# Performance work log

Hardware: AMD Instinct MI355X
Metric: run time of the kernel (lower is better)

Reference implementation:

```python
import jax, jax.numpy as jnp
import numpy as np

HEADS = 8
KEY_DIM = 64
VALUE_DIM = 64


def setup_inputs() -> dict:
    key = jax.random.key(0)
    ks = jax.random.split(key, 6)
    B, I, O, T, S = 2, 512, 512, 2048, 2048
    E = KEY_DIM * HEADS  # 512
    Ev = VALUE_DIM * HEADS  # 512
    return {
        "x": jax.random.normal(ks[0], (B, I, T), dtype=jnp.float32),
        "y": jax.random.normal(ks[1], (B, O, S), dtype=jnp.float32),
        "mask": jnp.zeros((T, S), dtype=jnp.float32),
        "Wk": jax.random.normal(ks[2], (E, I), dtype=jnp.float32) * (I ** -0.5),
        "Wv": jax.random.normal(ks[3], (Ev, I), dtype=jnp.float32) * (I ** -0.5),
        "Wq": jax.random.normal(ks[4], (E, O), dtype=jnp.float32) * (O ** -0.5),
        "W": jax.random.normal(ks[5], (O, Ev), dtype=jnp.float32) * (Ev ** -0.5),
        "b": jnp.zeros((O,), dtype=jnp.float32),
    }


def reference(x, y, mask, Wk, Wv, Wq, W, b):
    B, I, T = x.shape
    S = y.shape[2]
    H, dk, dv = HEADS, KEY_DIM, VALUE_DIM
    scaling = dk ** -0.5
    # 1x1 Conv1d projections == channel GEMMs; reshape (B, H*d, L) -> (B*H, d, L)
    keys = jnp.einsum('ei,bit->bet', Wk, x).reshape(B * H, dk, T)
    values = jnp.einsum('ei,bit->bet', Wv, x).reshape(B * H, dv, T)
    queries = jnp.einsum('eo,bos->bes', Wq, y).reshape(B * H, dk, S)
    # scores: [B*H, T, S]
    dot = jnp.einsum('bkt,bks->bts', keys, queries)
    dot = dot + mask[None, :, :]
    # torch Softmax(1) on [bh, T, S] normalizes over T (keys axis);
    # note: scaling applied AFTER mask add, as in the original.
    attention = jax.nn.softmax(scaling * dot, axis=1)
    # weighted values: [B*H, dv, S] -> [B, H*dv, S]
    output = jnp.einsum('bvt,bts->bvs', values, attention).reshape(B, H * dv, S)
    # final Linear over channel dim applied to (B, S, H*dv)
    return jnp.einsum('bvs,ov->bso', output, W) + b
```

## Files before the change

kernel.cpp:

```cpp
#include <hip/hip_runtime.h>
#include <stdint.h>

typedef unsigned short u16;
typedef unsigned int u32;

#define B_    2
#define DK    64
#define T_    2048
#define S_    2048
#define CI    512
#define CO    512
#define E_    512

typedef short  short8 __attribute__((ext_vector_type(8)));
typedef __bf16 bf16x8 __attribute__((ext_vector_type(8)));
typedef float  f32x4  __attribute__((ext_vector_type(4)));

static __device__ __forceinline__ u16 f2bf(float f) {
    return __builtin_bit_cast(u16, (__bf16)f);
}

static __device__ __forceinline__ float bf2f(u16 h) {
    return __uint_as_float((u32)h << 16);
}

static __device__ __forceinline__ short8 ld8(const u16* p) {
    return *(const short8*)p;
}

static __device__ __forceinline__ f32x4 mfma_bf16(short8 a, short8 b, f32x4 c) {
    return __builtin_amdgcn_mfma_f32_16x16x32_bf16(
        __builtin_bit_cast(bf16x8, a), __builtin_bit_cast(bf16x8, b), c, 0, 0, 0);
}

__global__ __launch_bounds__(256) void k_prep(const float* __restrict__ x, const float* __restrict__ y,
                                              const float* __restrict__ wk, const float* __restrict__ wv,
                                              const float* __restrict__ wq, const float* __restrict__ wf,
                                              const float* __restrict__ mask,
                                              u16* __restrict__ xt, u16* __restrict__ yt,
                                              u16* __restrict__ wkb, u16* __restrict__ wvb,
                                              u16* __restrict__ wqb, u16* __restrict__ wfb,
                                              u16* __restrict__ mt, u32* __restrict__ mflag) {
    __shared__ float tile[64][65];
    int bid = blockIdx.x;
    if (bid < 1024) {
        int bx = bid & 31, by = (bid >> 5) & 7, bz = bid >> 8;
        int tsel = bz >> 1, b = bz & 1;
        const float* src = tsel ? y : x;
        u16* dst = tsel ? yt : xt;
        int t0 = bx * 64, i0 = by * 64;
        int tx = threadIdx.x & 15, ty = threadIdx.x >> 4;
#pragma unroll
        for (int r = 0; r < 4; r++) {
            int i = ty + r * 16;
            *(float4*)&tile[i][tx * 4] =
                *(const float4*)(src + (size_t)(b * CI + i0 + i) * T_ + t0 + tx * 4);
        }
        __syncthreads();
        int tx2 = threadIdx.x & 7, ty2 = threadIdx.x >> 3;
#pragma unroll
        for (int r = 0; r < 2; r++) {
            int t = ty2 + r * 32;
            short8 o;
#pragma unroll
            for (int j = 0; j < 8; j++)
                o[j] = (short)f2bf(tile[tx2 * 8 + j][t]);
            *(short8*)(dst + (size_t)(b * T_ + t0 + t) * CI + i0 + tx2 * 8) = o;
        }
    } else if (bid < 1536) {
        int off = ((bid - 1024) * 256 + threadIdx.x) * 8;
        int w = off >> 18, r = off & 262143;
        const float* s = (w == 0) ? wk : (w == 1) ? wv : (w == 2) ? wq : wf;
        u16* d = (w == 0) ? wkb : (w == 1) ? wvb : (w == 2) ? wqb : wfb;
        float4 a0 = *(const float4*)(s + r);
        float4 a1 = *(const float4*)(s + r + 4);
        short8 o;
        o[0] = f2bf(a0.x); o[1] = f2bf(a0.y); o[2] = f2bf(a0.z); o[3] = f2bf(a0.w);
        o[4] = f2bf(a1.x); o[5] = f2bf(a1.y); o[6] = f2bf(a1.z); o[7] = f2bf(a1.w);
        *(short8*)(d + r) = o;
    } else {
        int mb = bid - 1536;
        int bx = mb & 31, by = mb >> 5;
        int t0 = bx * 64, s0 = by * 64;
        int tx = threadIdx.x & 15, ty = threadIdx.x >> 4;
        const float msc = 0.125f * 1.44269504088896f;
        bool nz = false;
#pragma unroll
        for (int r = 0; r < 4; r++) {
            int t = ty + r * 16;
            float4 v = *(const float4*)(mask + (size_t)(t0 + t) * S_ + s0 + tx * 4);
            nz |= (v.x != 0.0f) | (v.y != 0.0f) | (v.z != 0.0f) | (v.w != 0.0f);
            *(float4*)&tile[t][tx * 4] = v;
        }
        if (mflag && __any(nz) && (threadIdx.x & 63) == 0)
            atomicOr(mflag, 1u);
        __syncthreads();
        int tx2 = threadIdx.x & 7, ty2 = threadIdx.x >> 3;
#pragma unroll
        for (int r = 0; r < 2; r++) {
            int s = ty2 + r * 32;
            short8 o;
#pragma unroll
            for (int j = 0; j < 8; j++)
                o[j] = (short)f2bf(tile[tx2 * 8 + j][s] * msc);
            *(short8*)(mt + (size_t)(s0 + s) * T_ + t0 + tx2 * 8) = o;
        }
    }
}

__global__ __launch_bounds__(256) void k_proj3(const u16* __restrict__ xt, const u16* __restrict__ yt,
                                               const u16* __restrict__ wkb, const u16* __restrict__ wvb,
                                               const u16* __restrict__ wqb,
                                               u16* __restrict__ ktd, u16* __restrict__ vtd,
                                               u16* __restrict__ qtd, int p_base) {
    int bi = blockIdx.x;
    int p = p_base + (bi >> 8);
    int r = bi & 255;
    int et = r & 3, tt = r >> 2;
    int wv = threadIdx.x >> 6, lane = threadIdx.x & 63;
    int col = lane & 15, q = lane >> 4;
    int b = tt >> 5;
    int t0 = (tt & 31) * 64 + (wv >> 1) * 32;
    int e0 = et * 128 + (wv & 1) * 64;
    const u16* src = (p == 0) ? yt : xt;
    const u16* wb  = (p == 0) ? wqb : (p == 1) ? wkb : wvb;
    const u16* ap0 = src + (size_t)(b * T_ + t0 + col) * CI + q * 8;
    const u16* bp0 = wb + (size_t)(e0 + col) * CI + q * 8;
    f32x4 acc[2][4] = {};
    short8 a0 = ld8(ap0), a1 = ld8(ap0 + 16 * CI);
    short8 b0 = ld8(bp0), b1 = ld8(bp0 + 16 * CI);
    short8 b2 = ld8(bp0 + 32 * CI), b3 = ld8(bp0 + 48 * CI);
#pragma unroll
    for (int ks = 0; ks < 16; ks++) {
        short8 na0, na1, nb0, nb1, nb2, nb3;
        if (ks < 15) {
            na0 = ld8(ap0 + (ks + 1) * 32);
            na1 = ld8(ap0 + 16 * CI + (ks + 1) * 32);
            nb0 = ld8(bp0 + (ks + 1) * 32);
            nb1 = ld8(bp0 + 16 * CI + (ks + 1) * 32);
            nb2 = ld8(bp0 + 32 * CI + (ks + 1) * 32);
            nb3 = ld8(bp0 + 48 * CI + (ks + 1) * 32);
        }
        acc[0][0] = mfma_bf16(a0, b0, acc[0][0]); acc[1][0] = mfma_bf16(a1, b0, acc[1][0]);
        acc[0][1] = mfma_bf16(a0, b1, acc[0][1]); acc[1][1] = mfma_bf16(a1, b1, acc[1][1]);
        acc[0][2] = mfma_bf16(a0, b2, acc[0][2]); acc[1][2] = mfma_bf16(a1, b2, acc[1][2]);
        acc[0][3] = mfma_bf16(a0, b3, acc[0][3]); acc[1][3] = mfma_bf16(a1, b3, acc[1][3]);
        if (ks < 15) {
            a0 = na0; a1 = na1; b0 = nb0; b1 = nb1; b2 = nb2; b3 = nb3;
        }
    }
    float qs = (p == 0) ? 0.180336880f : 1.0f;
    u16* dst = (p == 0) ? qtd : (p == 1) ? ktd : vtd;
    if (p < 2) {
#pragma unroll
        for (int mt = 0; mt < 2; mt++)
#pragma unroll
            for (int nt = 0; nt < 4; nt++) {
                int e = e0 + nt * 16 + col, h = e >> 6, k = e & 63;
                u16* dp = dst + ((size_t)(b * 8 + h) * T_ + t0 + mt * 16 + q * 4) * DK + k;
                dp[0] = f2bf(acc[mt][nt][0] * qs);
                dp[DK] = f2bf(acc[mt][nt][1] * qs);
                dp[2 * DK] = f2bf(acc[mt][nt][2] * qs);
                dp[3 * DK] = f2bf(acc[mt][nt][3] * qs);
            }
    } else {
#pragma unroll
        for (int mt = 0; mt < 2; mt++)
#pragma unroll
            for (int nt = 0; nt < 4; nt++) {
                int e = e0 + nt * 16 + col, h = e >> 6, v = e & 63;
                uint2 pk;
                pk.x = f2bf(acc[mt][nt][0]) | ((u32)f2bf(acc[mt][nt][1]) << 16);
                pk.y = f2bf(acc[mt][nt][2]) | ((u32)f2bf(acc[mt][nt][3]) << 16);
                *(uint2*)(dst + ((size_t)(b * 8 + h) * DK + v) * T_ + t0 + mt * 16 + q * 4) = pk;
            }
    }
}


#define ATTN_ITER_M(T0, KC, MC4, MCF, KN, MN4, MNF, TN)  do {                       \
    short8 vb0 = ld8(vbase + (T0));                                                 \
    short8 vb1 = ld8(vbase + 16 * (size_t)T_ + (T0));                               \
    short8 vb2 = ld8(vbase + 32 * (size_t)T_ + (T0));                               \
    short8 vb3 = ld8(vbase + 48 * (size_t)T_ + (T0));                               \
    f32x4 s0g[4], s1g[4];                                                           \
    __builtin_amdgcn_s_setprio(1);                                                  \
    _Pragma("unroll") for (int g = 0; g < 4; g++) {                                 \
        f32x4 z = {};                                                               \
        s0g[g] = mfma_bf16(KC[0], qa[g][0], z);                                     \
        s0g[g] = mfma_bf16(KC[1], qa[g][1], s0g[g]);                                \
        s1g[g] = mfma_bf16(KC[2], qa[g][0], z);                                     \
        s1g[g] = mfma_bf16(KC[3], qa[g][1], s1g[g]);                                \
    }                                                                               \
    __builtin_amdgcn_s_setprio(0);                                                  \
    KN[0] = ld8(kbase + (size_t)(TN) * DK);                                         \
    KN[1] = ld8(kbase + (size_t)(TN) * DK + 32);                                    \
    KN[2] = ld8(kbase + (size_t)((TN) + 4) * DK);                                   \
    KN[3] = ld8(kbase + (size_t)((TN) + 4) * DK + 32);                              \
    if constexpr (MODE == 1) {                                                      \
        _Pragma("unroll") for (int g = 0; g < 4; g++) {                             \
            MN4[g][0] = *(const ushort4*)(mtb[g] + (TN));                           \
            MN4[g][1] = *(const ushort4*)(mtb[g] + (TN) + 4);                       \
        }                                                                           \
    } else {                                                                        \
        _Pragma("unroll") for (int g = 0; g < 4; g++)                               \
        _Pragma("unroll") for (int st = 0; st < 2; st++)                            \
        _Pragma("unroll") for (int rr = 0; rr < 4; rr++)                            \
            MNF[g][st * 4 + rr] =                                                   \
                mbs[g][(size_t)((TN) + q * 8 + st * 4 + rr) * S_] * msc;            \
    }                                                                               \
    _Pragma("unroll") for (int g = 0; g < 4; g++) {                                 \
        bf16x8 pbv;                                                                 \
        float lsum = 0.f;                                                           \
        _Pragma("unroll") for (int i = 0; i < 8; i++) {                             \
            float sv = (i < 4) ? s0g[g][i & 3] : s1g[g][i & 3];                     \
            float mv;                                                               \
            if constexpr (MODE == 1)                                                \
                mv = bf2f(((const u16*)&MC4[g][i >> 2])[i & 3]);                    \
            else                                                                    \
                mv = MCF[g][i];                                                     \
            float p = __builtin_amdgcn_exp2f(sv + mv);                              \
            lsum += p;                                                              \
            pbv[i] = (__bf16)p;                                                     \
        }                                                                           \
        l_part[g] += lsum;                                                          \
        short8 pa = __builtin_bit_cast(short8, pbv);                                \
        __builtin_amdgcn_s_setprio(1);                                              \
        oacc[g][0] = mfma_bf16(vb0, pa, oacc[g][0]);                                \
        oacc[g][1] = mfma_bf16(vb1, pa, oacc[g][1]);                                \
        oacc[g][2] = mfma_bf16(vb2, pa, oacc[g][2]);                                \
        oacc[g][3] = mfma_bf16(vb3, pa, oacc[g][3]);                                \
        __builtin_amdgcn_s_setprio(0);                                              \
    }                                                                               \
} while (0)

#define ATTN_ITER_NM(T0, KC, KN, TN)  do {                                          \
    short8 vb0 = ld8(vbase + (T0));                                                 \
    short8 vb1 = ld8(vbase + 16 * (size_t)T_ + (T0));                               \
    short8 vb2 = ld8(vbase + 32 * (size_t)T_ + (T0));                               \
    short8 vb3 = ld8(vbase + 48 * (size_t)T_ + (T0));                               \
    f32x4 s0g[4], s1g[4];                                                           \
    __builtin_amdgcn_s_setprio(1);                                                  \
    _Pragma("unroll") for (int g = 0; g < 4; g++) {                                 \
        f32x4 z = {};                                                               \
        s0g[g] = mfma_bf16(KC[0], qa[g][0], z);                                     \
        s0g[g] = mfma_bf16(KC[1], qa[g][1], s0g[g]);                                \
        s1g[g] = mfma_bf16(KC[2], qa[g][0], z);                                     \
        s1g[g] = mfma_bf16(KC[3], qa[g][1], s1g[g]);                                \
    }                                                                               \
    __builtin_amdgcn_s_setprio(0);                                                  \
    KN[0] = ld8(kbase + (size_t)(TN) * DK);                                         \
    KN[1] = ld8(kbase + (size_t)(TN) * DK + 32);                                    \
    KN[2] = ld8(kbase + (size_t)((TN) + 4) * DK);                                   \
    KN[3] = ld8(kbase + (size_t)((TN) + 4) * DK + 32);                              \
    _Pragma("unroll") for (int g = 0; g < 4; g++) {                                 \
        bf16x8 pbv;                                                                 \
        float lsum = 0.f;                                                           \
        _Pragma("unroll") for (int i = 0; i < 8; i++) {                             \
            float sv = (i < 4) ? s0g[g][i & 3] : s1g[g][i & 3];                     \
            float p = __builtin_amdgcn_exp2f(sv);                                   \
            lsum += p;                                                              \
            pbv[i] = (__bf16)p;                                                     \
        }                                                                           \
        l_part[g] += lsum;                                                          \
        short8 pa = __builtin_bit_cast(short8, pbv);                                \
        __builtin_amdgcn_s_setprio(1);                                              \
        oacc[g][0] = mfma_bf16(vb0, pa, oacc[g][0]);                                \
        oacc[g][1] = mfma_bf16(vb1, pa, oacc[g][1]);                                \
        oacc[g][2] = mfma_bf16(vb2, pa, oacc[g][2]);                                \
        oacc[g][3] = mfma_bf16(vb3, pa, oacc[g][3]);                                \
        __builtin_amdgcn_s_setprio(0);                                              \
    }                                                                               \
} while (0)

template<int MODE>
__global__ __launch_bounds__(512, 2) void k_attn(const u16* __restrict__ kt, const u16* __restrict__ qt,
                                                 const u16* __restrict__ vt, const float* __restrict__ mask,
                                                 const u16* __restrict__ mt, const u32* __restrict__ mflag,
                                                 u16* __restrict__ oa) {
    __shared__ struct { float O[8][16][68]; float L[8][16]; } Sm;
    int wv = threadIdx.x >> 6, lane = threadIdx.x & 63;
    int col = lane & 15, q = lane >> 4;
    int bid = blockIdx.x;
    int j = bid >> 3;
    int bh = (bid & 7) * 2 + (j >> 5);
    int s_base = (j & 31) * 64;
    int sg = s_base + col;
    const int t_begin = wv * (T_ / 8);
    const int t_end = t_begin + (T_ / 8);
    short8 qa[4][2];
#pragma unroll
    for (int g = 0; g < 4; g++) {
        const u16* qp = qt + (size_t)(bh * S_ + sg + g * 16) * DK + q * 8;
        qa[g][0] = ld8(qp);
        qa[g][1] = ld8(qp + 32);
    }
    int tperm = ((col >> 2) << 3) | (col & 3);
    const u16* kbase = kt + (size_t)bh * T_ * DK + (size_t)tperm * DK + q * 8;
    const u16* vbase = vt + (size_t)bh * DK * T_ + (size_t)col * T_ + q * 8;
    float l_part[4] = {0.f, 0.f, 0.f, 0.f};
    f32x4 oacc[4][4] = {};
    const float msc = 0.180336880f;

    int use_mask = mflag ? (int)*mflag : 1;

    if (use_mask == 0) {
        short8 kA[4], kB[4];
        kA[0] = ld8(kbase + (size_t)t_begin * DK);
        kA[1] = ld8(kbase + (size_t)t_begin * DK + 32);
        kA[2] = ld8(kbase + (size_t)(t_begin + 4) * DK);
        kA[3] = ld8(kbase + (size_t)(t_begin + 4) * DK + 32);
        for (int t0 = t_begin; t0 < t_end; t0 += 64) {
            ATTN_ITER_NM(t0, kA, kB, t0 + 32);
            int tn2 = (t0 + 64 < t_end) ? (t0 + 64) : t_begin;
            ATTN_ITER_NM(t0 + 32, kB, kA, tn2);
        }
    } else {
        const float* mbs[4];
        const u16* mtb[4];
#pragma unroll
        for (int g = 0; g < 4; g++) {
            mbs[g] = mask + sg + g * 16;
            mtb[g] = mt + (size_t)(sg + g * 16) * T_ + q * 8;
        }
        short8 kA[4], kB[4];
        ushort4 mA4[4][2], mB4[4][2];
        float mAf[4][8], mBf[4][8];
        kA[0] = ld8(kbase + (size_t)t_begin * DK);
        kA[1] = ld8(kbase + (size_t)t_begin * DK + 32);
        kA[2] = ld8(kbase + (size_t)(t_begin + 4) * DK);
        kA[3] = ld8(kbase + (size_t)(t_begin + 4) * DK + 32);
        if constexpr (MODE == 1) {
#pragma unroll
            for (int g = 0; g < 4; g++) {
                mA4[g][0] = *(const ushort4*)(mtb[g] + t_begin);
                mA4[g][1] = *(const ushort4*)(mtb[g] + t_begin + 4);
            }
        } else {
#pragma unroll
            for (int g = 0; g < 4; g++)
#pragma unroll
                for (int st = 0; st < 2; st++)
#pragma unroll
                    for (int rr = 0; rr < 4; rr++)
                        mAf[g][st * 4 + rr] =
                            mbs[g][(size_t)(t_begin + q * 8 + st * 4 + rr) * S_] * msc;
        }
        for (int t0 = t_begin; t0 < t_end; t0 += 64) {
            ATTN_ITER_M(t0, kA, mA4, mAf, kB, mB4, mBf, t0 + 32);
            int tn2 = (t0 + 64 < t_end) ? (t0 + 64) : t_begin;
            ATTN_ITER_M(t0 + 32, kB, mB4, mBf, kA, mA4, mAf, tn2);
        }
    }

#pragma unroll
    for (int g = 0; g < 4; g++) {
        float lr = l_part[g];
        lr += __shfl_xor(lr, 16);
        lr += __shfl_xor(lr, 32);
        l_part[g] = lr;
    }

    int b = bh >> 3, h = bh & 7;
    __syncthreads();
#pragma unroll
    for (int g = 0; g < 4; g++) {
#pragma unroll
        for (int nt = 0; nt < 4; nt++)
            *(f32x4*)&Sm.O[wv][col][nt * 16 + q * 4] = oacc[g][nt];
        if (lane < 16)
            Sm.L[wv][lane] = l_part[g];
        __syncthreads();
#pragma unroll
        for (int e = 0; e < 2; e++) {
            int f = (int)threadIdx.x + e * 512;
            int s = f >> 6, v = f & 63;
            float acc = 0.f, lt = 0.f;
#pragma unroll
            for (int c = 0; c < 8; c++) {
                acc += Sm.O[c][s][v];
                lt += Sm.L[c][s];
            }
            oa[(size_t)(b * S_ + s_base + g * 16 + s) * E_ + h * DK + v] = f2bf(acc / lt);
        }
        __syncthreads();
    }
}

__global__ __launch_bounds__(256) void k_final(const u16* __restrict__ oa, const u16* __restrict__ wfb,
                                               const float* __restrict__ bias, float* __restrict__ out) {
    int bi = blockIdx.x;
    int et = bi & 7, tt = bi >> 3;
    int wv = threadIdx.x >> 6, lane = threadIdx.x & 63;
    int col = lane & 15, q = lane >> 4;
    int b = tt >> 5;
    int s0 = (tt & 31) * 64 + (wv >> 1) * 32;
    int o0 = et * 64 + (wv & 1) * 32;
    const u16* ap0 = oa + (size_t)(b * S_ + s0 + col) * E_ + q * 8;
    const u16* bp0 = wfb + (size_t)(o0 + col) * E_ + q * 8;
    f32x4 acc[2][2] = {};
    short8 a0 = ld8(ap0), a1 = ld8(ap0 + 16 * E_);
    short8 b0 = ld8(bp0), b1 = ld8(bp0 + 16 * E_);
#pragma unroll
    for (int ks = 0; ks < 16; ks++) {
        short8 na0, na1, nb0, nb1;
        if (ks < 15) {
            na0 = ld8(ap0 + (ks + 1) * 32);
            na1 = ld8(ap0 + 16 * E_ + (ks + 1) * 32);
            nb0 = ld8(bp0 + (ks + 1) * 32);
            nb1 = ld8(bp0 + 16 * E_ + (ks + 1) * 32);
        }
        acc[0][0] = mfma_bf16(a0, b0, acc[0][0]); acc[1][0] = mfma_bf16(a1, b0, acc[1][0]);
        acc[0][1] = mfma_bf16(a0, b1, acc[0][1]); acc[1][1] = mfma_bf16(a1, b1, acc[1][1]);
        if (ks < 15) {
            a0 = na0; a1 = na1; b0 = nb0; b1 = nb1;
        }
    }
#pragma unroll
    for (int mt = 0; mt < 2; mt++)
#pragma unroll
        for (int nt = 0; nt < 2; nt++) {
            int o = o0 + nt * 16 + col;
            float bn = bias[o];
#pragma unroll
            for (int r = 0; r < 4; r++) {
                int s = s0 + mt * 16 + q * 4 + r;
                out[(size_t)(b * S_ + s) * CO + o] = acc[mt][nt][r] + bn;
            }
        }
}

extern "C" void kernel_launch(void* const* d_in, const int* in_sizes, int n_in,
                              void* d_out, int out_size, void* d_ws, size_t ws_size,
                              hipStream_t stream) {
    const float* x    = (const float*)d_in[0];
    const float* y    = (const float*)d_in[1];
    const float* mask = (const float*)d_in[2];
    const float* Wk   = (const float*)d_in[3];
    const float* Wv   = (const float*)d_in[4];
    const float* Wq   = (const float*)d_in[5];
    const float* Wf   = (const float*)d_in[6];
    const float* bias = (const float*)d_in[7];
    float* out = (float*)d_out;

    u16* ws = (u16*)d_ws;
    u16* XT  = ws;
    u16* YT  = XT + 2097152;
    u16* WKB = YT + 2097152;
    u16* WVB = WKB + 262144;
    u16* WQB = WVB + 262144;
    u16* WFB = WQB + 262144;
    u16* KT  = WFB + 262144;
    u16* QT  = KT + 2097152;
    u16* MT  = QT + 2097152;
    u16* VTs = MT + 4194304;
    u32* MF  = (u32*)(VTs + 2097152);
    u16* OA  = XT;

    int use_mt   = (ws_size >= (size_t)27262976) ? 1 : 0;
    int has_vt   = (ws_size >= (size_t)31457280) ? 1 : 0;
    int has_flag = (ws_size >= (size_t)31457344) ? 1 : 0;
    u16* VT = has_vt ? VTs : YT;
    u32* MFp = (use_mt && has_flag) ? MF : (u32*)nullptr;

    if (MFp)
        hipMemsetAsync(MFp, 0, 4, stream);
    k_prep<<<use_mt ? 2560 : 1536, 256, 0, stream>>>(x, y, Wk, Wv, Wq, Wf, mask,
                                                     XT, YT, WKB, WVB, WQB, WFB, MT, MFp);
    if (has_vt) {
        k_proj3<<<768, 256, 0, stream>>>(XT, YT, WKB, WVB, WQB, KT, VT, QT, 0);
    } else {
        k_proj3<<<512, 256, 0, stream>>>(XT, YT, WKB, WVB, WQB, KT, VT, QT, 0);
        k_proj3<<<256, 256, 0, stream>>>(XT, YT, WKB, WVB, WQB, KT, VT, QT, 2);
    }
    if (use_mt)
        k_attn<1><<<512, 512, 0, stream>>>(KT, QT, VT, mask, MT, MFp, OA);
    else
        k_attn<0><<<512, 512, 0, stream>>>(KT, QT, VT, mask, MT, MFp, OA);
    k_final<<<512, 256, 0, stream>>>(OA, WFB, bias, out);
}
```

Measured before the change: 195.5 us.

## Store K and V in MFMA fragment-major layout for contiguous attention loads

The projection kernel now writes K and V in a pre-swizzled fragment layout: per 32-row t-tile and per 16-byte register fragment, all 64 lanes' data sit contiguously. The attention kernel then loads each K/V fragment as one fully coalesced 1 KB wave-wide read at lane*8, instead of strided per-row gathers with a tperm permutation. This is meant to cut memory transactions and address arithmetic in the attention inner loop. In exchange the projection kernel does scattered 2-byte stores for K and small uint2 stores for V into the swizzled layout.

```diff
diff --git a/kernel.cpp b/kernel.cpp
--- a/kernel.cpp
+++ b/kernel.cpp
@@ -111,7 +111,7 @@
 __global__ __launch_bounds__(256) void k_proj3(const u16* __restrict__ xt, const u16* __restrict__ yt,
                                                const u16* __restrict__ wkb, const u16* __restrict__ wvb,
                                                const u16* __restrict__ wqb,
-                                               u16* __restrict__ ktd, u16* __restrict__ vtd,
+                                               u16* __restrict__ kfd, u16* __restrict__ vfd,
                                                u16* __restrict__ qtd, int p_base) {
     int bi = blockIdx.x;
     int p = p_base + (bi >> 8);
@@ -149,40 +149,60 @@
             a0 = na0; a1 = na1; b0 = nb0; b1 = nb1; b2 = nb2; b3 = nb3;
         }
     }
-    float qs = (p == 0) ? 0.180336880f : 1.0f;
-    u16* dst = (p == 0) ? qtd : (p == 1) ? ktd : vtd;
-    if (p < 2) {
+    const float qs = 0.180336880f;
+    if (p == 0) {
 #pragma unroll
         for (int mt = 0; mt < 2; mt++)
 #pragma unroll
             for (int nt = 0; nt < 4; nt++) {
                 int e = e0 + nt * 16 + col, h = e >> 6, k = e & 63;
-                u16* dp = dst + ((size_t)(b * 8 + h) * T_ + t0 + mt * 16 + q * 4) * DK + k;
+                u16* dp = qtd + ((size_t)(b * 8 + h) * T_ + t0 + mt * 16 + q * 4) * DK + k;
                 dp[0] = f2bf(acc[mt][nt][0] * qs);
                 dp[DK] = f2bf(acc[mt][nt][1] * qs);
                 dp[2 * DK] = f2bf(acc[mt][nt][2] * qs);
                 dp[3 * DK] = f2bf(acc[mt][nt][3] * qs);
             }
+    } else if (p == 1) {
+        int ttk = t0 >> 5;
+#pragma unroll
+        for (int mt = 0; mt < 2; mt++) {
+            int cb = (mt * 2 + (q >> 1)) << 2;
+#pragma unroll
+            for (int nt = 0; nt < 4; nt++) {
+                int e = e0 + nt * 16 + col, h = e >> 6, k = e & 63;
+                int pp = ((q & 1) << 1) | (k >> 5);
+                int lf = (((k & 31) >> 3) << 4) + cb;
+                u16* dp = kfd + ((((size_t)(b * 8 + h) * 64 + ttk) * 4 + pp) * 64 + lf) * 8 + (k & 7);
+                dp[0]  = f2bf(acc[mt][nt][0]);
+                dp[8]  = f2bf(acc[mt][nt][1]);
+                dp[16] = f2bf(acc[mt][nt][2]);
+                dp[24] = f2bf(acc[mt][nt][3]);
+            }
+        }
     } else {
-#pragma unroll
-        for (int mt = 0; mt < 2; mt++)
+        int ttv = t0 >> 5;
+        int j0 = (q & 1) * 4;
+#pragma unroll
+        for (int mt = 0; mt < 2; mt++) {
+            int lf = col | ((mt * 2 + (q >> 1)) << 4);
 #pragma unroll
             for (int nt = 0; nt < 4; nt++) {
-                int e = e0 + nt * 16 + col, h = e >> 6, v = e & 63;
+                int e = e0 + nt * 16 + col, h = e >> 6;
                 uint2 pk;
                 pk.x = f2bf(acc[mt][nt][0]) | ((u32)f2bf(acc[mt][nt][1]) << 16);
                 pk.y = f2bf(acc[mt][nt][2]) | ((u32)f2bf(acc[mt][nt][3]) << 16);
-                *(uint2*)(dst + ((size_t)(b * 8 + h) * DK + v) * T_ + t0 + mt * 16 + q * 4) = pk;
+                *(uint2*)(vfd + ((((size_t)(b * 8 + h) * 64 + ttv) * 4 + nt) * 64 + lf) * 8 + j0) = pk;
             }
-    }
-}
-
-
-#define ATTN_ITER_M(T0, KC, MC4, MCF, KN, MN4, MNF, TN)  do {                       \
-    short8 vb0 = ld8(vbase + (T0));                                                 \
-    short8 vb1 = ld8(vbase + 16 * (size_t)T_ + (T0));                               \
-    short8 vb2 = ld8(vbase + 32 * (size_t)T_ + (T0));                               \
-    short8 vb3 = ld8(vbase + 48 * (size_t)T_ + (T0));                               \
+        }
+    }
+}
+
+
+#define ATTN_ITER_M(TT, KC, MC4, MCF, KN, MN4, MNF, TTN)  do {                      \
+    short8 vb0 = ld8(vfb + ((TT) * 4 + 0) * 512);                                   \
+    short8 vb1 = ld8(vfb + ((TT) * 4 + 1) * 512);                                   \
+    short8 vb2 = ld8(vfb + ((TT) * 4 + 2) * 512);                                   \
+    short8 vb3 = ld8(vfb + ((TT) * 4 + 3) * 512);                                   \
     f32x4 s0g[4], s1g[4];                                                           \
     __builtin_amdgcn_s_setprio(1);                                                  \
     _Pragma("unroll") for (int g = 0; g < 4; g++) {                                 \
@@ -193,21 +213,21 @@
         s1g[g] = mfma_bf16(KC[3], qa[g][1], s1g[g]);                                \
     }                                                                               \
     __builtin_amdgcn_s_setprio(0);                                                  \
-    KN[0] = ld8(kbase + (size_t)(TN) * DK);                                         \
-    KN[1] = ld8(kbase + (size_t)(TN) * DK + 32);                                    \
-    KN[2] = ld8(kbase + (size_t)((TN) + 4) * DK);                                   \
-    KN[3] = ld8(kbase + (size_t)((TN) + 4) * DK + 32);                              \
+    KN[0] = ld8(kfb + ((TTN) * 4 + 0) * 512);                                       \
+    KN[1] = ld8(kfb + ((TTN) * 4 + 1) * 512);                                       \
+    KN[2] = ld8(kfb + ((TTN) * 4 + 2) * 512);                                       \
+    KN[3] = ld8(kfb + ((TTN) * 4 + 3) * 512);                                       \
     if constexpr (MODE == 1) {                                                      \
         _Pragma("unroll") for (int g = 0; g < 4; g++) {                             \
-            MN4[g][0] = *(const ushort4*)(mtb[g] + (TN));                           \
-            MN4[g][1] = *(const ushort4*)(mtb[g] + (TN) + 4);                       \
+            MN4[g][0] = *(const ushort4*)(mtb[g] + (TTN) * 32);                     \
+            MN4[g][1] = *(const ushort4*)(mtb[g] + (TTN) * 32 + 4);                 \
         }                                                                           \
     } else {                                                                        \
         _Pragma("unroll") for (int g = 0; g < 4; g++)                               \
         _Pragma("unroll") for (int st = 0; st < 2; st++)                            \
         _Pragma("unroll") for (int rr = 0; rr < 4; rr++)                            \
             MNF[g][st * 4 + rr] =                                                   \
-                mbs[g][(size_t)((TN) + q * 8 + st * 4 + rr) * S_] * msc;            \
+                mbs[g][(size_t)((TTN) * 32 + q * 8 + st * 4 + rr) * S_] * msc;      \
     }                                                                               \
     _Pragma("unroll") for (int g = 0; g < 4; g++) {                                 \
         bf16x8 pbv;                                                                 \
@@ -234,11 +254,11 @@
     }                                                                               \
 } while (0)
 
-#define ATTN_ITER_NM(T0, KC, KN, TN)  do {                                          \
-    short8 vb0 = ld8(vbase + (T0));                                                 \
-    short8 vb1 = ld8(vbase + 16 * (size_t)T_ + (T0));                               \
-    short8 vb2 = ld8(vbase + 32 * (size_t)T_ + (T0));                               \
-    short8 vb3 = ld8(vbase + 48 * (size_t)T_ + (T0));                               \
+#define ATTN_ITER_NM(TT, KC, KN, TTN)  do {                                         \
+    short8 vb0 = ld8(vfb + ((TT) * 4 + 0) * 512);                                   \
+    short8 vb1 = ld8(vfb + ((TT) * 4 + 1) * 512);                                   \
+    short8 vb2 = ld8(vfb + ((TT) * 4 + 2) * 512);                                   \
+    short8 vb3 = ld8(vfb + ((TT) * 4 + 3) * 512);                                   \
     f32x4 s0g[4], s1g[4];                                                           \
     __builtin_amdgcn_s_setprio(1);                                                  \
     _Pragma("unroll") for (int g = 0; g < 4; g++) {                                 \
@@ -249,10 +269,10 @@
         s1g[g] = mfma_bf16(KC[3], qa[g][1], s1g[g]);                                \
     }                                                                               \
     __builtin_amdgcn_s_setprio(0);                                                  \
-    KN[0] = ld8(kbase + (size_t)(TN) * DK);                                         \
-    KN[1] = ld8(kbase + (size_t)(TN) * DK + 32);                                    \
-    KN[2] = ld8(kbase + (size_t)((TN) + 4) * DK);                                   \
-    KN[3] = ld8(kbase + (size_t)((TN) + 4) * DK + 32);                              \
+    KN[0] = ld8(kfb + ((TTN) * 4 + 0) * 512);                                       \
+    KN[1] = ld8(kfb + ((TTN) * 4 + 1) * 512);                                       \
+    KN[2] = ld8(kfb + ((TTN) * 4 + 2) * 512);                                       \
+    KN[3] = ld8(kfb + ((TTN) * 4 + 3) * 512);                                       \
     _Pragma("unroll") for (int g = 0; g < 4; g++) {                                 \
         bf16x8 pbv;                                                                 \
         float lsum = 0.f;                                                           \
@@ -274,8 +294,8 @@
 } while (0)
 
 template<int MODE>
-__global__ __launch_bounds__(512, 2) void k_attn(const u16* __restrict__ kt, const u16* __restrict__ qt,
-                                                 const u16* __restrict__ vt, const float* __restrict__ mask,
+__global__ __launch_bounds__(512, 2) void k_attn(const u16* __restrict__ kf, const u16* __restrict__ qt,
+                                                 const u16* __restrict__ vf, const float* __restrict__ mask,
                                                  const u16* __restrict__ mt, const u32* __restrict__ mflag,
                                                  u16* __restrict__ oa) {
     __shared__ struct { float O[8][16][68]; float L[8][16]; } Sm;
@@ -286,8 +306,8 @@
     int bh = (bid & 7) * 2 + (j >> 5);
     int s_base = (j & 31) * 64;
     int sg = s_base + col;
-    const int t_begin = wv * (T_ / 8);
-    const int t_end = t_begin + (T_ / 8);
+    const int tt_begin = wv * 8;
+    const int tt_end = tt_begin + 8;
     short8 qa[4][2];
 #pragma unroll
     for (int g = 0; g < 4; g++) {
@@ -295,9 +315,8 @@
         qa[g][0] = ld8(qp);
         qa[g][1] = ld8(qp + 32);
     }
-    int tperm = ((col >> 2) << 3) | (col & 3);
-    const u16* kbase = kt + (size_t)bh * T_ * DK + (size_t)tperm * DK + q * 8;
-    const u16* vbase = vt + (size_t)bh * DK * T_ + (size_t)col * T_ + q * 8;
+    const u16* kfb = kf + (size_t)bh * 131072 + lane * 8;
+    const u16* vfb = vf + (size_t)bh * 131072 + lane * 8;
     float l_part[4] = {0.f, 0.f, 0.f, 0.f};
     f32x4 oacc[4][4] = {};
     const float msc = 0.180336880f;
@@ -306,14 +325,14 @@
 
     if (use_mask == 0) {
         short8 kA[4], kB[4];
-        kA[0] = ld8(kbase + (size_t)t_begin * DK);
-        kA[1] = ld8(kbase + (size_t)t_begin * DK + 32);
-        kA[2] = ld8(kbase + (size_t)(t_begin + 4) * DK);
-        kA[3] = ld8(kbase + (size_t)(t_begin + 4) * DK + 32);
-        for (int t0 = t_begin; t0 < t_end; t0 += 64) {
-            ATTN_ITER_NM(t0, kA, kB, t0 + 32);
-            int tn2 = (t0 + 64 < t_end) ? (t0 + 64) : t_begin;
-            ATTN_ITER_NM(t0 + 32, kB, kA, tn2);
+        kA[0] = ld8(kfb + (tt_begin * 4 + 0) * 512);
+        kA[1] = ld8(kfb + (tt_begin * 4 + 1) * 512);
+        kA[2] = ld8(kfb + (tt_begin * 4 + 2) * 512);
+        kA[3] = ld8(kfb + (tt_begin * 4 + 3) * 512);
+        for (int tt = tt_begin; tt < tt_end; tt += 2) {
+            ATTN_ITER_NM(tt, kA, kB, tt + 1);
+            int ttn2 = (tt + 2 < tt_end) ? (tt + 2) : tt_begin;
+            ATTN_ITER_NM(tt + 1, kB, kA, ttn2);
         }
     } else {
         const float* mbs[4];
@@ -326,15 +345,15 @@
         short8 kA[4], kB[4];
         ushort4 mA4[4][2], mB4[4][2];
         float mAf[4][8], mBf[4][8];
-        kA[0] = ld8(kbase + (size_t)t_begin * DK);
-        kA[1] = ld8(kbase + (size_t)t_begin * DK + 32);
-        kA[2] = ld8(kbase + (size_t)(t_begin + 4) * DK);
-        kA[3] = ld8(kbase + (size_t)(t_begin + 4) * DK + 32);
+        kA[0] = ld8(kfb + (tt_begin * 4 + 0) * 512);
+        kA[1] = ld8(kfb + (tt_begin * 4 + 1) * 512);
+        kA[2] = ld8(kfb + (tt_begin * 4 + 2) * 512);
+        kA[3] = ld8(kfb + (tt_begin * 4 + 3) * 512);
         if constexpr (MODE == 1) {
 #pragma unroll
             for (int g = 0; g < 4; g++) {
-                mA4[g][0] = *(const ushort4*)(mtb[g] + t_begin);
-                mA4[g][1] = *(const ushort4*)(mtb[g] + t_begin + 4);
+                mA4[g][0] = *(const ushort4*)(mtb[g] + tt_begin * 32);
+                mA4[g][1] = *(const ushort4*)(mtb[g] + tt_begin * 32 + 4);
             }
         } else {
 #pragma unroll
@@ -344,12 +363,12 @@
 #pragma unroll
                     for (int rr = 0; rr < 4; rr++)
                         mAf[g][st * 4 + rr] =
-                            mbs[g][(size_t)(t_begin + q * 8 + st * 4 + rr) * S_] * msc;
-        }
-        for (int t0 = t_begin; t0 < t_end; t0 += 64) {
-            ATTN_ITER_M(t0, kA, mA4, mAf, kB, mB4, mBf, t0 + 32);
-            int tn2 = (t0 + 64 < t_end) ? (t0 + 64) : t_begin;
-            ATTN_ITER_M(t0 + 32, kB, mB4, mBf, kA, mA4, mAf, tn2);
+                            mbs[g][(size_t)(tt_begin * 32 + q * 8 + st * 4 + rr) * S_] * msc;
+        }
+        for (int tt = tt_begin; tt < tt_end; tt += 2) {
+            ATTN_ITER_M(tt, kA, mA4, mAf, kB, mB4, mBf, tt + 1);
+            int ttn2 = (tt + 2 < tt_end) ? (tt + 2) : tt_begin;
+            ATTN_ITER_M(tt + 1, kB, mB4, mBf, kA, mA4, mAf, ttn2);
         }
     }
 
@@ -450,32 +469,32 @@
     u16* WVB = WKB + 262144;
     u16* WQB = WVB + 262144;
     u16* WFB = WQB + 262144;
-    u16* KT  = WFB + 262144;
-    u16* QT  = KT + 2097152;
+    u16* KF  = WFB + 262144;
+    u16* QT  = KF + 2097152;
     u16* MT  = QT + 2097152;
-    u16* VTs = MT + 4194304;
-    u32* MF  = (u32*)(VTs + 2097152);
+    u16* VFs = MT + 4194304;
+    u32* MF  = (u32*)(VFs + 2097152);
     u16* OA  = XT;
 
     int use_mt   = (ws_size >= (size_t)27262976) ? 1 : 0;
     int has_vt   = (ws_size >= (size_t)31457280) ? 1 : 0;
     int has_flag = (ws_size >= (size_t)31457344) ? 1 : 0;
-    u16* VT = has_vt ? VTs : YT;
+    u16* VF = has_vt ? VFs : YT;
     u32* MFp = (use_mt && has_flag) ? MF : (u32*)nullptr;
 
     if (MFp)
-        hipMemsetAsync(MFp, 0, 4, stream);
+        (void)hipMemsetAsync(MFp, 0, 4, stream);
     k_prep<<<use_mt ? 2560 : 1536, 256, 0, stream>>>(x, y, Wk, Wv, Wq, Wf, mask,
                                                      XT, YT, WKB, WVB, WQB, WFB, MT, MFp);
     if (has_vt) {
-        k_proj3<<<768, 256, 0, stream>>>(XT, YT, WKB, WVB, WQB, KT, VT, QT, 0);
+        k_proj3<<<768, 256, 0, stream>>>(XT, YT, WKB, WVB, WQB, KF, VF, QT, 0);
     } else {
-        k_proj3<<<512, 256, 0, stream>>>(XT, YT, WKB, WVB, WQB, KT, VT, QT, 0);
-        k_proj3<<<256, 256, 0, stream>>>(XT, YT, WKB, WVB, WQB, KT, VT, QT, 2);
+        k_proj3<<<512, 256, 0, stream>>>(XT, YT, WKB, WVB, WQB, KF, VF, QT, 0);
+        k_proj3<<<256, 256, 0, stream>>>(XT, YT, WKB, WVB, WQB, KF, VF, QT, 2);
     }
     if (use_mt)
-        k_attn<1><<<512, 512, 0, stream>>>(KT, QT, VT, mask, MT, MFp, OA);
+        k_attn<1><<<512, 512, 0, stream>>>(KF, QT, VF, mask, MT, MFp, OA);
     else
-        k_attn<0><<<512, 512, 0, stream>>>(KT, QT, VT, mask, MT, MFp, OA);
+        k_attn<0><<<512, 512, 0, stream>>>(KF, QT, VF, mask, MT, MFp, OA);
     k_final<<<512, 256, 0, stream>>>(OA, WFB, bias, out);
 }
```

Measured after the change: 171.2 us. 12.4% less time.
